# Kernel tuning notes

Hardware: AMD Instinct MI355X
Metric: run time of the kernel (lower is better)

## Reference

```python
import jax, jax.numpy as jnp
import numpy as np

N_BINS = 15


def setup_inputs() -> dict:
    key = jax.random.key(0)
    k1, k2 = jax.random.split(key)
    N, C = 1000000, 100
    logits = jax.random.normal(k1, (N, C), dtype=jnp.float32)
    labels = jax.random.randint(k2, (N,), 0, C, dtype=jnp.int64)
    return {"logits": logits, "labels": labels, "t_opt": 0}


def reference(logits, labels, t_opt):
    # temperature scaling branch (t_opt is a static Python int)
    scaled = logits / t_opt if t_opt != 0 else logits
    probs = jax.nn.softmax(scaled, axis=-1)            # [N, C]
    confidences = jnp.max(probs, axis=1)               # [N]
    predictions = jnp.argmax(probs, axis=1)            # [N]
    accuracies = (predictions == labels).astype(jnp.float32)

    # bin index: confidences in (bin_lower, bin_upper] -> single-pass histogram
    boundaries = jnp.linspace(0.0, 1.0, N_BINS + 1)
    bin_idx = jnp.clip(
        jnp.searchsorted(boundaries, confidences, side="left") - 1, 0, N_BINS - 1
    )

    ones = jnp.ones_like(confidences)
    counts = jax.ops.segment_sum(ones, bin_idx, num_segments=N_BINS)
    sum_conf = jax.ops.segment_sum(confidences, bin_idx, num_segments=N_BINS)
    sum_acc = jax.ops.segment_sum(accuracies, bin_idx, num_segments=N_BINS)

    n = confidences.shape[0]
    safe = jnp.maximum(counts, 1.0)
    avg_conf = sum_conf / safe
    avg_acc = sum_acc / safe
    prop = counts / n
    per_bin = jnp.where(counts > 0, jnp.abs(avg_conf - avg_acc) * prop, 0.0)
    return jnp.sum(per_bin).reshape(1)
```

## Files before the change

kernel.cpp:

```cpp
#include <hip/hip_runtime.h>
#include <math.h>

#define NBINS 15
#define CROWS 16
#define F4C   (CROWS * 25)
#define BLOCK 256
#define WPB   (BLOCK / 64)

typedef float nat_f4 __attribute__((ext_vector_type(4)));

__device__ __forceinline__ void compute_chunk(
    const float4* __restrict__ buf, int r, int q, long long rbase, int labCur,
    float scale, int N, float* s_cnt, float* s_conf, float* s_acc)
{
    if (rbase + r >= N) return;
    const float4* rowp = buf + r * 25;
    const int nf = (q == 0) ? 7 : 6;
    const int fb = (q == 0) ? 0 : (1 + q * 6);

    float4 v[7];
#pragma unroll
    for (int j = 0; j < 7; ++j)
        if (j < nf) v[j] = rowp[fb + j];

    float m = -INFINITY; int mi = 0;
#pragma unroll
    for (int j = 0; j < 7; ++j) if (j < nf) {
        const int cb = (fb + j) * 4;
        float4 w = v[j];
        w.x *= scale; w.y *= scale; w.z *= scale; w.w *= scale;
        v[j] = w;
        if (w.x > m) { m = w.x; mi = cb;     }
        if (w.y > m) { m = w.y; mi = cb + 1; }
        if (w.z > m) { m = w.z; mi = cb + 2; }
        if (w.w > m) { m = w.w; mi = cb + 3; }
    }
#pragma unroll
    for (int off = 1; off <= 2; off <<= 1) {
        const float om  = __shfl_xor(m, off);
        const int   omi = __shfl_xor(mi, off);
        if (om > m || (om == m && omi < mi)) { m = om; mi = omi; }
    }

    float e = 0.f;
#pragma unroll
    for (int j = 0; j < 7; ++j) if (j < nf) {
        const float4 w = v[j];
        e += __expf(w.x - m) + __expf(w.y - m)
           + __expf(w.z - m) + __expf(w.w - m);
    }
    e += __shfl_xor(e, 1);
    e += __shfl_xor(e, 2);

    if (q == 0) {
        const float conf = 1.0f / e;
        const float acc  = (mi == labCur) ? 1.0f : 0.0f;
        int jc = 0;
#pragma unroll
        for (int i = 0; i <= NBINS; ++i) {
            const float b = (float)i * (1.0f / 15.0f);
            jc += (b < conf) ? 1 : 0;
        }
        int bin = jc - 1;
        bin = bin < 0 ? 0 : (bin > NBINS - 1 ? NBINS - 1 : bin);
        atomicAdd(&s_cnt[bin],  1.0f);
        atomicAdd(&s_conf[bin], conf);
        atomicAdd(&s_acc[bin],  acc);
    }
}

__global__ __launch_bounds__(BLOCK, 3) void ece_main(const float* __restrict__ logits,
                                                     const int* __restrict__ labels,
                                                     const int* __restrict__ t_opt,
                                                     float* __restrict__ gbins,
                                                     int N) {
    __shared__ float4 s_tile[WPB][2][F4C];
    __shared__ float s_cnt[NBINS], s_conf[NBINS], s_acc[NBINS];

    const int tid  = threadIdx.x;
    const int lane = tid & 63;
    const int wv   = tid >> 6;
    const int r    = lane >> 2;
    const int q    = lane & 3;

    if (tid < NBINS) { s_cnt[tid] = 0.f; s_conf[tid] = 0.f; s_acc[tid] = 0.f; }
    __syncthreads();

    const int tt = t_opt[0];
    float scale = (tt != 0) ? (1.0f / (float)tt) : 1.0f;
    asm volatile("" :: "v"(scale));

    const nat_f4* __restrict__ lg4 = (const nat_f4*)logits;
    const int limF4   = N * 25 - 1;
    const int nChunks = (N + CROWS - 1) / CROWS;
    const int stride  = gridDim.x * WPB;

    nat_f4 sA0, sA1, sA2, sA3, sA4, sA5, sA6;  int labsA = 0;
    nat_f4 sB0, sB1, sB2, sB3, sB4, sB5, sB6;  int labsB = 0;

#define CLK(k) ((k) < limF4 ? (k) : limF4)
#define ISSUE(P, cc) do {                                                     \
    const int b_ = (cc) * F4C + lane;                                         \
    P##0 = __builtin_nontemporal_load(lg4 + CLK(b_));                         \
    P##1 = __builtin_nontemporal_load(lg4 + CLK(b_ + 64));                    \
    P##2 = __builtin_nontemporal_load(lg4 + CLK(b_ + 128));                   \
    P##3 = __builtin_nontemporal_load(lg4 + CLK(b_ + 192));                   \
    P##4 = __builtin_nontemporal_load(lg4 + CLK(b_ + 256));                   \
    P##5 = __builtin_nontemporal_load(lg4 + CLK(b_ + 320));                   \
    if (lane < 16) P##6 = __builtin_nontemporal_load(lg4 + CLK(b_ + 384));    \
    if (q == 0) { const int rr_ = (cc) * CROWS + r;                           \
                  lab##P = __builtin_nontemporal_load(                        \
                               labels + (rr_ < N ? rr_ : N - 1)); }           \
} while (0)

#define DSW(P, b) do {                                                        \
    nat_f4* d_ = (nat_f4*)&s_tile[wv][b][lane];                               \
    d_[0]   = P##0; d_[64]  = P##1; d_[128] = P##2;                           \
    d_[192] = P##3; d_[256] = P##4; d_[320] = P##5;                           \
    if (lane < 16) d_[384] = P##6;                                            \
} while (0)

#define VMW8  asm volatile("s_waitcnt vmcnt(8)" ::: "memory")
#define VMW0  asm volatile("s_waitcnt vmcnt(0)" ::: "memory")
#define LGKM0 asm volatile("s_waitcnt lgkmcnt(0)" ::: "memory")
#define SBR   __builtin_amdgcn_sched_barrier(0)

    int  c     = blockIdx.x * WPB + wv;
    bool vCur  = (c < nChunks);
    bool vNext = (c + stride < nChunks);
    int  cur   = 0;

    if (vCur)  ISSUE(sA, c);
    if (vNext) ISSUE(sB, c + stride);
    if (vCur) {
        if (vNext) VMW8; else VMW0;
        SBR;
        DSW(sA, 0);
        LGKM0; SBR;
    }

    if (vCur) for (;;) {
        {
            const int  cn2 = c + 2 * stride;
            const bool v2  = cn2 < nChunks;
            const int  labCur = labsA;
            if (v2) ISSUE(sA, cn2);
            compute_chunk(&s_tile[wv][cur][0], r, q, (long long)c * CROWS,
                          labCur, scale, N, s_cnt, s_conf, s_acc);
            if (vNext) {
                if (v2) VMW8; else VMW0;
                SBR;
                DSW(sB, cur ^ 1);
                LGKM0; SBR;
            }
            vCur = vNext; vNext = v2; c += stride; cur ^= 1;
            if (!vCur) break;
        }
        {
            const int  cn2 = c + 2 * stride;
            const bool v2  = cn2 < nChunks;
            const int  labCur = labsB;
            if (v2) ISSUE(sB, cn2);
            compute_chunk(&s_tile[wv][cur][0], r, q, (long long)c * CROWS,
                          labCur, scale, N, s_cnt, s_conf, s_acc);
            if (vNext) {
                if (v2) VMW8; else VMW0;
                SBR;
                DSW(sA, cur ^ 1);
                LGKM0; SBR;
            }
            vCur = vNext; vNext = v2; c += stride; cur ^= 1;
            if (!vCur) break;
        }
    }

    VMW0;
    __syncthreads();
    if (tid < NBINS) {
        atomicAdd(&gbins[tid],             s_cnt[tid]);
        atomicAdd(&gbins[NBINS + tid],     s_conf[tid]);
        atomicAdd(&gbins[2 * NBINS + tid], s_acc[tid]);
    }
#undef CLK
#undef ISSUE
#undef DSW
#undef VMW8
#undef VMW0
#undef LGKM0
#undef SBR
}

__global__ void ece_final(const float* __restrict__ gbins,
                          float* __restrict__ out, int N) {
    if (threadIdx.x == 0 && blockIdx.x == 0) {
        float ece = 0.f;
        for (int b = 0; b < NBINS; ++b) {
            const float c = gbins[b];
            if (c > 0.f) {
                const float avg_conf = gbins[NBINS + b] / c;
                const float avg_acc  = gbins[2 * NBINS + b] / c;
                ece += fabsf(avg_conf - avg_acc) * (c / (float)N);
            }
        }
        out[0] = ece;
    }
}

extern "C" void kernel_launch(void* const* d_in, const int* in_sizes, int n_in,
                              void* d_out, int out_size, void* d_ws, size_t ws_size,
                              hipStream_t stream) {
    const float* logits = (const float*)d_in[0];
    const int*   labels = (const int*)d_in[1];
    const int*   t_opt  = (const int*)d_in[2];
    float* out   = (float*)d_out;
    float* gbins = (float*)d_ws;

    const int N = in_sizes[1];

    hipMemsetAsync(gbins, 0, 3 * NBINS * sizeof(float), stream);

    const int nChunks = (N + CROWS - 1) / CROWS;
    int blocks = (nChunks + WPB - 1) / WPB;
    if (blocks > 768) blocks = 768;
    ece_main<<<blocks, BLOCK, 0, stream>>>(logits, labels, t_opt, gbins, N);
    ece_final<<<1, 64, 0, stream>>>(gbins, out, N);
}
```

Before: 87.19 us.

## Halve rows per wave chunk, use 8 lanes per row, double occupancy

Each wave now processes 8 rows per chunk instead of 16, with 8 lanes cooperating per row, so each lane holds 3-4 float4s instead of 6-7. The prefetch register sets shrink, the vmcnt wait threshold drops to match the smaller load count, launch bounds rise to 6 waves per SIMD, and the grid cap doubles to 1536 blocks. The goal is more waves in flight to hide HBM latency in a bandwidth-bound pass. In exchange it adds an extra shuffle stage to each reduction, makes a higher share of lanes idle during the histogram step, and gives more loop iterations per byte loaded.

```diff
diff --git a/kernel.cpp b/kernel.cpp
--- a/kernel.cpp
+++ b/kernel.cpp
@@ -2,7 +2,7 @@
 #include <math.h>
 
 #define NBINS 15
-#define CROWS 16
+#define CROWS 8
 #define F4C   (CROWS * 25)
 #define BLOCK 256
 #define WPB   (BLOCK / 64)
@@ -15,17 +15,17 @@
 {
     if (rbase + r >= N) return;
     const float4* rowp = buf + r * 25;
-    const int nf = (q == 0) ? 7 : 6;
-    const int fb = (q == 0) ? 0 : (1 + q * 6);
-
-    float4 v[7];
-#pragma unroll
-    for (int j = 0; j < 7; ++j)
+    const int nf = (q == 0) ? 4 : 3;
+    const int fb = (q == 0) ? 0 : (1 + 3 * q);
+
+    float4 v[4];
+#pragma unroll
+    for (int j = 0; j < 4; ++j)
         if (j < nf) v[j] = rowp[fb + j];
 
     float m = -INFINITY; int mi = 0;
 #pragma unroll
-    for (int j = 0; j < 7; ++j) if (j < nf) {
+    for (int j = 0; j < 4; ++j) if (j < nf) {
         const int cb = (fb + j) * 4;
         float4 w = v[j];
         w.x *= scale; w.y *= scale; w.z *= scale; w.w *= scale;
@@ -36,7 +36,7 @@
         if (w.w > m) { m = w.w; mi = cb + 3; }
     }
 #pragma unroll
-    for (int off = 1; off <= 2; off <<= 1) {
+    for (int off = 1; off <= 4; off <<= 1) {
         const float om  = __shfl_xor(m, off);
         const int   omi = __shfl_xor(mi, off);
         if (om > m || (om == m && omi < mi)) { m = om; mi = omi; }
@@ -44,13 +44,14 @@
 
     float e = 0.f;
 #pragma unroll
-    for (int j = 0; j < 7; ++j) if (j < nf) {
+    for (int j = 0; j < 4; ++j) if (j < nf) {
         const float4 w = v[j];
         e += __expf(w.x - m) + __expf(w.y - m)
            + __expf(w.z - m) + __expf(w.w - m);
     }
     e += __shfl_xor(e, 1);
     e += __shfl_xor(e, 2);
+    e += __shfl_xor(e, 4);
 
     if (q == 0) {
         const float conf = 1.0f / e;
@@ -69,7 +70,7 @@
     }
 }
 
-__global__ __launch_bounds__(BLOCK, 3) void ece_main(const float* __restrict__ logits,
+__global__ __launch_bounds__(BLOCK, 6) void ece_main(const float* __restrict__ logits,
                                                      const int* __restrict__ labels,
                                                      const int* __restrict__ t_opt,
                                                      float* __restrict__ gbins,
@@ -80,8 +81,8 @@
     const int tid  = threadIdx.x;
     const int lane = tid & 63;
     const int wv   = tid >> 6;
-    const int r    = lane >> 2;
-    const int q    = lane & 3;
+    const int r    = lane >> 3;
+    const int q    = lane & 7;
 
     if (tid < NBINS) { s_cnt[tid] = 0.f; s_conf[tid] = 0.f; s_acc[tid] = 0.f; }
     __syncthreads();
@@ -95,8 +96,8 @@
     const int nChunks = (N + CROWS - 1) / CROWS;
     const int stride  = gridDim.x * WPB;
 
-    nat_f4 sA0, sA1, sA2, sA3, sA4, sA5, sA6;  int labsA = 0;
-    nat_f4 sB0, sB1, sB2, sB3, sB4, sB5, sB6;  int labsB = 0;
+    nat_f4 sA0, sA1, sA2, sA3;  int labsA = 0;
+    nat_f4 sB0, sB1, sB2, sB3;  int labsB = 0;
 
 #define CLK(k) ((k) < limF4 ? (k) : limF4)
 #define ISSUE(P, cc) do {                                                     \
@@ -104,10 +105,7 @@
     P##0 = __builtin_nontemporal_load(lg4 + CLK(b_));                         \
     P##1 = __builtin_nontemporal_load(lg4 + CLK(b_ + 64));                    \
     P##2 = __builtin_nontemporal_load(lg4 + CLK(b_ + 128));                   \
-    P##3 = __builtin_nontemporal_load(lg4 + CLK(b_ + 192));                   \
-    P##4 = __builtin_nontemporal_load(lg4 + CLK(b_ + 256));                   \
-    P##5 = __builtin_nontemporal_load(lg4 + CLK(b_ + 320));                   \
-    if (lane < 16) P##6 = __builtin_nontemporal_load(lg4 + CLK(b_ + 384));    \
+    if (lane < 8) P##3 = __builtin_nontemporal_load(lg4 + CLK(b_ + 192));     \
     if (q == 0) { const int rr_ = (cc) * CROWS + r;                           \
                   lab##P = __builtin_nontemporal_load(                        \
                                labels + (rr_ < N ? rr_ : N - 1)); }           \
@@ -115,12 +113,11 @@
 
 #define DSW(P, b) do {                                                        \
     nat_f4* d_ = (nat_f4*)&s_tile[wv][b][lane];                               \
-    d_[0]   = P##0; d_[64]  = P##1; d_[128] = P##2;                           \
-    d_[192] = P##3; d_[256] = P##4; d_[320] = P##5;                           \
-    if (lane < 16) d_[384] = P##6;                                            \
+    d_[0] = P##0; d_[64] = P##1; d_[128] = P##2;                              \
+    if (lane < 8) d_[192] = P##3;                                             \
 } while (0)
 
-#define VMW8  asm volatile("s_waitcnt vmcnt(8)" ::: "memory")
+#define VMW5  asm volatile("s_waitcnt vmcnt(5)" ::: "memory")
 #define VMW0  asm volatile("s_waitcnt vmcnt(0)" ::: "memory")
 #define LGKM0 asm volatile("s_waitcnt lgkmcnt(0)" ::: "memory")
 #define SBR   __builtin_amdgcn_sched_barrier(0)
@@ -133,7 +130,7 @@
     if (vCur)  ISSUE(sA, c);
     if (vNext) ISSUE(sB, c + stride);
     if (vCur) {
-        if (vNext) VMW8; else VMW0;
+        if (vNext) VMW5; else VMW0;
         SBR;
         DSW(sA, 0);
         LGKM0; SBR;
@@ -145,10 +142,11 @@
             const bool v2  = cn2 < nChunks;
             const int  labCur = labsA;
             if (v2) ISSUE(sA, cn2);
-            compute_chunk(&s_tile[wv][cur][0], r, q, (long long)c * CROWS,
-                          labCur, scale, N, s_cnt, s_conf, s_acc);
+            compute_chunk((const float4*)&s_tile[wv][cur][0], r, q,
+                          (long long)c * CROWS, labCur, scale, N,
+                          s_cnt, s_conf, s_acc);
             if (vNext) {
-                if (v2) VMW8; else VMW0;
+                if (v2) VMW5; else VMW0;
                 SBR;
                 DSW(sB, cur ^ 1);
                 LGKM0; SBR;
@@ -161,10 +159,11 @@
             const bool v2  = cn2 < nChunks;
             const int  labCur = labsB;
             if (v2) ISSUE(sB, cn2);
-            compute_chunk(&s_tile[wv][cur][0], r, q, (long long)c * CROWS,
-                          labCur, scale, N, s_cnt, s_conf, s_acc);
+            compute_chunk((const float4*)&s_tile[wv][cur][0], r, q,
+                          (long long)c * CROWS, labCur, scale, N,
+                          s_cnt, s_conf, s_acc);
             if (vNext) {
-                if (v2) VMW8; else VMW0;
+                if (v2) VMW5; else VMW0;
                 SBR;
                 DSW(sA, cur ^ 1);
                 LGKM0; SBR;
@@ -184,7 +183,7 @@
 #undef CLK
 #undef ISSUE
 #undef DSW
-#undef VMW8
+#undef VMW5
 #undef VMW0
 #undef LGKM0
 #undef SBR
@@ -221,7 +220,7 @@
 
     const int nChunks = (N + CROWS - 1) / CROWS;
     int blocks = (nChunks + WPB - 1) / WPB;
-    if (blocks > 768) blocks = 768;
+    if (blocks > 1536) blocks = 1536;
     ece_main<<<blocks, BLOCK, 0, stream>>>(logits, labels, t_opt, gbins, N);
     ece_final<<<1, 64, 0, stream>>>(gbins, out, N);
 }
```

New measurement: 135.5 us. 55.4% more time.
